# Kernel optimization log

Measured on AMD Instinct MI355X. Metric: run time of the kernel, lower is better.

The kernel has to match this reference:

```python
import jax, jax.numpy as jnp
import numpy as np

H, CM, CS = 8, 16, 32  # num_heads, hidden_mv_channels, hidden_s_channels
_INNER_IDX = np.array([0, 2, 3, 4, 8, 9, 10, 14])  # PGA multivector components without e0


def _make_basis():
    # 9 Pin(3,0,1)-equivariant linear maps on 16-dim multivectors:
    # 5 grade projections + 4 left-multiplications by e0 (grade k -> grade k+1 e0-blades).
    # Component order: [1, e0, e1, e2, e3, e01, e02, e03, e12, e13, e23, e012, e013, e023, e123, e0123]
    b = np.zeros((9, 16, 16), dtype=np.float32)
    grades = [[0], [1, 2, 3, 4], [5, 6, 7, 8, 9, 10], [11, 12, 13, 14], [15]]
    for k, idxs in enumerate(grades):
        for i in idxs:
            b[k, i, i] = 1.0
    e0maps = {5: [(0, 1)], 6: [(2, 5), (3, 6), (4, 7)], 7: [(8, 11), (9, 12), (10, 13)], 8: [(14, 15)]}
    for k, pairs in e0maps.items():
        for i, o in pairs:
            b[k, o, i] = 1.0
    return jnp.asarray(b)


BASIS = _make_basis()  # (9, 16_out_comp, 16_in_comp)


def equi_linear(mv, s, w_mv, w_s2mv, b_mv, w_mv2s, w_s2s, b_s):
    # mv: (..., c_in, 16); s: (..., s_in)
    out_mv = jnp.einsum('yai,ocy,...ci->...oa', BASIS, w_mv, mv)
    out_mv = out_mv.at[..., 0].add(jnp.einsum('...i,oi->...o', s, w_s2mv) + b_mv)
    out_s = (jnp.einsum('...c,sc->...s', mv[..., 0], w_mv2s)
             + jnp.einsum('...i,si->...s', s, w_s2s) + b_s)
    return out_mv, out_s


def reference(multivectors_kv, multivectors_q, scalars_kv, scalars_q,
              q_w_mv, q_w_s2mv, q_b_mv, q_w_mv2s, q_w_s2s, q_b_s,
              k_w_mv, k_w_s2mv, k_b_mv, k_w_mv2s, k_w_s2s, k_b_s,
              v_w_mv, v_w_s2mv, v_b_mv, v_w_mv2s, v_w_s2s, v_b_s,
              o_w_mv, o_w_s2mv, o_b_mv, o_w_mv2s, o_w_s2s, o_b_s):
    B, Q = multivectors_q.shape[0], multivectors_q.shape[1]
    q_mv, q_s = equi_linear(multivectors_q, scalars_q, q_w_mv, q_w_s2mv, q_b_mv, q_w_mv2s, q_w_s2s, q_b_s)
    k_mv, k_s = equi_linear(multivectors_kv, scalars_kv, k_w_mv, k_w_s2mv, k_b_mv, k_w_mv2s, k_w_s2s, k_b_s)
    v_mv, v_s = equi_linear(multivectors_kv, scalars_kv, v_w_mv, v_w_s2mv, v_b_mv, v_w_mv2s, v_w_s2s, v_b_s)
    # split heads; einops pattern '(hidden_channels num_heads)' => channel-major, head-minor
    q_mv = q_mv.reshape(B, Q, CM, H, 16).transpose(0, 3, 1, 2, 4)  # (B,H,Q,CM,16)
    q_s = q_s.reshape(B, Q, CS, H).transpose(0, 3, 1, 2)            # (B,H,Q,CS)
    # multi-query: single k/v head broadcast over H
    scale = 1.0 / jnp.sqrt(jnp.asarray(8 * CM + CS, dtype=q_mv.dtype))
    scores = (jnp.einsum('bhqcx,bkcx->bhqk', q_mv[..., _INNER_IDX], k_mv[..., _INNER_IDX])
              + jnp.einsum('bhqs,bks->bhqk', q_s, k_s)) * scale
    attn = jax.nn.softmax(scores, axis=-1)
    h_mv = jnp.einsum('bhqk,bkcx->bhqcx', attn, v_mv)
    h_s = jnp.einsum('bhqk,bkc->bhqc', attn, v_s)
    # merge heads; pattern '(n_heads hidden_channels)' => head-major
    h_mv = h_mv.transpose(0, 2, 1, 3, 4).reshape(B, Q, H * CM, 16)
    h_s = h_s.transpose(0, 2, 1, 3).reshape(B, Q, H * CS)
    out_mv, out_s = equi_linear(h_mv, h_s, o_w_mv, o_w_s2mv, o_b_mv, o_w_mv2s, o_w_s2s, o_b_s)
    return out_mv, out_s


def setup_inputs():
    key = jax.random.key(0)
    ks = jax.random.split(key, 32)
    B, NQ, NKV, IN_MV, IN_S = 4, 2048, 2048, 16, 32
    w = 0.05  # weight scale to keep attention logits sane

    def rn(k, shape, s=1.0):
        return jax.random.normal(k, shape, dtype=jnp.float32) * s

    return {
        'multivectors_kv': rn(ks[0], (B, NKV, IN_MV, 16)),
        'multivectors_q': rn(ks[1], (B, NQ, IN_MV, 16)),
        'scalars_kv': rn(ks[2], (B, NKV, IN_S)),
        'scalars_q': rn(ks[3], (B, NQ, IN_S)),
        'q_w_mv': rn(ks[4], (CM * H, IN_MV, 9), w),
        'q_w_s2mv': rn(ks[5], (CM * H, IN_S), w),
        'q_b_mv': jnp.zeros((CM * H,), jnp.float32),
        'q_w_mv2s': rn(ks[6], (CS * H, IN_MV), w),
        'q_w_s2s': rn(ks[7], (CS * H, IN_S), w),
        'q_b_s': jnp.zeros((CS * H,), jnp.float32),
        'k_w_mv': rn(ks[8], (CM, IN_MV, 9), w),
        'k_w_s2mv': rn(ks[9], (CM, IN_S), w),
        'k_b_mv': jnp.zeros((CM,), jnp.float32),
        'k_w_mv2s': rn(ks[10], (CS, IN_MV), w),
        'k_w_s2s': rn(ks[11], (CS, IN_S), w),
        'k_b_s': jnp.zeros((CS,), jnp.float32),
        'v_w_mv': rn(ks[12], (CM, IN_MV, 9), w),
        'v_w_s2mv': rn(ks[13], (CM, IN_S), w),
        'v_b_mv': jnp.zeros((CM,), jnp.float32),
        'v_w_mv2s': rn(ks[14], (CS, IN_MV), w),
        'v_w_s2s': rn(ks[15], (CS, IN_S), w),
        'v_b_s': jnp.zeros((CS,), jnp.float32),
        'o_w_mv': rn(ks[16], (16, CM * H, 9), w),
        'o_w_s2mv': rn(ks[17], (16, CS * H), w),
        'o_b_mv': jnp.zeros((16,), jnp.float32),
        'o_w_mv2s': rn(ks[18], (32, CM * H), w),
        'o_w_s2s': rn(ks[19], (32, CS * H), w),
        'o_b_s': jnp.zeros((32,), jnp.float32),
    }
```

## Files before the change

### kernel.cpp

```cpp
#include <hip/hip_runtime.h>
#include <hip/hip_bf16.h>
#include <math.h>

#define NB   4
#define NQL  2048
#define NKVL 2048
#define HN   8
#define DQK  160
#define DV   288
#define QT   256
#define KTL  64
#define KLP  168

#define SCALE 0.07905694150420949f

typedef __attribute__((ext_vector_type(8)))  short short8;
typedef __attribute__((ext_vector_type(4)))  float f32x4;
typedef __attribute__((ext_vector_type(16))) float f32x16;

__constant__ int c_grade[16] = {0,1,1,1,1,2,2,2,2,2,2,3,3,3,3,4};
__constant__ int c_inner[8]  = {0,2,3,4,8,9,10,14};
__constant__ int c_esrc[16]  = {-1,0,-1,-1,-1,2,3,4,-1,-1,-1,8,9,10,-1,14};
__constant__ int c_ey[16]    = {0,5,0,0,0,6,6,6,0,0,0,7,7,7,0,8};

__device__ __forceinline__ ushort f2bf(float v) {
  __hip_bfloat16 h = __float2bfloat16(v);
  union { __hip_bfloat16 b; ushort u; } cv; cv.b = h; return cv.u;
}

__device__ __forceinline__ void gload16(const void* g, void* l) {
  __builtin_amdgcn_global_load_lds(
      (const __attribute__((address_space(1))) unsigned int*)g,
      (__attribute__((address_space(3))) unsigned int*)l, 16, 0, 0);
}

#define KWMV   0
#define KS2MV  2304
#define KMV2S  2816
#define KS2S   3328
#define KBMV   4352
#define KBS    4368
#define VWMV   4400
#define VS2MV  6704
#define VMV2S  7216
#define VS2S   7728
#define VBMV   8752
#define VBS    8768
#define WLSZ   8800
#define XSTR   289
#define OSTR   456
#define KVPOS  8

__device__ __forceinline__ void kv_accum(const float* wL, const float* xL,
                                         int f, float acc[KVPOS]) {
  if (f < 160) {
    if (f < 128) {
      int c = f >> 3, a = c_inner[f & 7], y = c_grade[a];
      float bias = (a == 0) ? wL[KBMV + c] : 0.f;
#pragma unroll
      for (int p = 0; p < KVPOS; p++) acc[p] = bias;
      for (int ci = 0; ci < 16; ci++) {
        float w = wL[KWMV + (c*16 + ci)*9 + y];
#pragma unroll
        for (int p = 0; p < KVPOS; p++) acc[p] += w * xL[p*XSTR + ci*16 + a];
      }
      if (a == 0) {
        for (int i2 = 0; i2 < 32; i2++) {
          float w = wL[KS2MV + c*32 + i2];
#pragma unroll
          for (int p = 0; p < KVPOS; p++) acc[p] += w * xL[p*XSTR + 256 + i2];
        }
      }
    } else {
      int si = f - 128;
      float bias = wL[KBS + si];
#pragma unroll
      for (int p = 0; p < KVPOS; p++) acc[p] = bias;
      for (int ci = 0; ci < 16; ci++) {
        float w = wL[KMV2S + si*16 + ci];
#pragma unroll
        for (int p = 0; p < KVPOS; p++) acc[p] += w * xL[p*XSTR + ci*16];
      }
      for (int i2 = 0; i2 < 32; i2++) {
        float w = wL[KS2S + si*32 + i2];
#pragma unroll
        for (int p = 0; p < KVPOS; p++) acc[p] += w * xL[p*XSTR + 256 + i2];
      }
    }
  } else {
    int g = f - 160;
    if (g < 256) {
      int c = g >> 4, a = g & 15, y = c_grade[a];
      float bias = (a == 0) ? wL[VBMV + c] : 0.f;
#pragma unroll
      for (int p = 0; p < KVPOS; p++) acc[p] = bias;
      for (int ci = 0; ci < 16; ci++) {
        float w = wL[VWMV + (c*16 + ci)*9 + y];
#pragma unroll
        for (int p = 0; p < KVPOS; p++) acc[p] += w * xL[p*XSTR + ci*16 + a];
      }
      int sa = c_esrc[a];
      if (sa >= 0) {
        int ey = c_ey[a];
        for (int ci = 0; ci < 16; ci++) {
          float w = wL[VWMV + (c*16 + ci)*9 + ey];
#pragma unroll
          for (int p = 0; p < KVPOS; p++) acc[p] += w * xL[p*XSTR + ci*16 + sa];
        }
      }
      if (a == 0) {
        for (int i2 = 0; i2 < 32; i2++) {
          float w = wL[VS2MV + c*32 + i2];
#pragma unroll
          for (int p = 0; p < KVPOS; p++) acc[p] += w * xL[p*XSTR + 256 + i2];
        }
      }
    } else {
      int si = g - 256;
      float bias = wL[VBS + si];
#pragma unroll
      for (int p = 0; p < KVPOS; p++) acc[p] = bias;
      for (int ci = 0; ci < 16; ci++) {
        float w = wL[VMV2S + si*16 + ci];
#pragma unroll
        for (int p = 0; p < KVPOS; p++) acc[p] += w * xL[p*XSTR + ci*16];
      }
      for (int i2 = 0; i2 < 32; i2++) {
        float w = wL[VS2S + si*32 + i2];
#pragma unroll
        for (int p = 0; p < KVPOS; p++) acc[p] += w * xL[p*XSTR + 256 + i2];
      }
    }
  }
}

__global__ __launch_bounds__(256) void proj_kv_kernel(
    const float* __restrict__ mv_kv, const float* __restrict__ s_kv,
    const float* __restrict__ kw_mv, const float* __restrict__ kw_s2mv, const float* __restrict__ kb_mv,
    const float* __restrict__ kw_mv2s, const float* __restrict__ kw_s2s, const float* __restrict__ kb_s,
    const float* __restrict__ vw_mv, const float* __restrict__ vw_s2mv, const float* __restrict__ vb_mv,
    const float* __restrict__ vw_mv2s, const float* __restrict__ vw_s2s, const float* __restrict__ vb_s,
    ushort* __restrict__ Kf, ushort* __restrict__ VfT)
{
  __shared__ float wL[WLSZ];
  __shared__ float xL[KVPOS*XSTR];
  int t = threadIdx.x;
  for (int i = t; i < 2304; i += 256) wL[KWMV + i] = kw_mv[i];
  for (int i = t; i < 512;  i += 256) wL[KS2MV + i] = kw_s2mv[i];
  for (int i = t; i < 512;  i += 256) wL[KMV2S + i] = kw_mv2s[i];
  for (int i = t; i < 1024; i += 256) wL[KS2S + i] = kw_s2s[i];
  if (t < 16) wL[KBMV + t] = kb_mv[t];
  if (t < 32) wL[KBS + t] = kb_s[t];
  for (int i = t; i < 2304; i += 256) wL[VWMV + i] = vw_mv[i];
  for (int i = t; i < 512;  i += 256) wL[VS2MV + i] = vw_s2mv[i];
  for (int i = t; i < 512;  i += 256) wL[VMV2S + i] = vw_mv2s[i];
  for (int i = t; i < 1024; i += 256) wL[VS2S + i] = vw_s2s[i];
  if (t < 16) wL[VBMV + t] = vb_mv[t];
  if (t < 32) wL[VBS + t] = vb_s[t];

  int p0 = blockIdx.x * KVPOS;
  for (int i = t; i < KVPOS*256; i += 256) {
    int p = i >> 8, c = i & 255;
    xL[p*XSTR + c] = mv_kv[(size_t)(p0 + p)*256 + c];
  }
  if (t < KVPOS*32) {
    int p = t >> 5, c = t & 31;
    xL[p*XSTR + 256 + c] = s_kv[(size_t)(p0 + p)*32 + c];
  }
  __syncthreads();

  float acc0[KVPOS], acc1[KVPOS];
  kv_accum(wL, xL, t, acc0);
  if (t < 192) kv_accum(wL, xL, 256 + t, acc1);
  __syncthreads();

  ushort* oL = (ushort*)xL;
#pragma unroll
  for (int p = 0; p < KVPOS; p++) oL[p*OSTR + t] = f2bf(acc0[p]);
  if (t < 192) {
#pragma unroll
    for (int p = 0; p < KVPOS; p++) oL[p*OSTR + 256 + t] = f2bf(acc1[p]);
  }
  __syncthreads();

  int b = p0 >> 11, kv0 = p0 & 2047;
  for (int it = 0; it < 3; it++) {
    int j = t + it*256;
    if (j < KVPOS*80) {
      int p = j / 80, fp = j - p*80;
      uint u = (uint)oL[p*OSTR + 2*fp] | ((uint)oL[p*OSTR + 2*fp + 1] << 16);
      *(uint*)(Kf + (size_t)(p0 + p)*DQK + 2*fp) = u;
    }
  }
  for (int it = 0; it < 5; it++) {
    int j = t + it*256;
    if (j < DV*(KVPOS/2)) {
      int g = j >> 2, pp = j & 3;
      uint u = (uint)oL[(2*pp)*OSTR + 160 + g] | ((uint)oL[(2*pp+1)*OSTR + 160 + g] << 16);
      int kv = kv0 + 2*pp;
      int pos = (kv & ~63) + ((((kv >> 3) & 7) ^ (g & 7)) << 3) + (kv & 7);
      *(uint*)(VfT + ((size_t)b*DV + g)*NKVL + pos) = u;
    }
  }
}

#define OWT_SZ 34816
#define QWT_MV 0
#define QWT_S  20480
#define QBT    61440
#define QWT_SZ 62720
__global__ __launch_bounds__(256) void prep_w_kernel(
    const float* __restrict__ ow_mv, const float* __restrict__ ow_s2mv,
    const float* __restrict__ ow_mv2s, const float* __restrict__ ow_s2s,
    float* __restrict__ owT,
    const float* __restrict__ qw_mv, const float* __restrict__ qw_s2mv, const float* __restrict__ qb_mv,
    const float* __restrict__ qw_mv2s, const float* __restrict__ qw_s2s, const float* __restrict__ qb_s,
    float* __restrict__ qwT)
{
  int i = blockIdx.x*256 + threadIdx.x;
  if (i < OWT_SZ) {
    if (i < 18432) {
      int y = i / 2048, r = i & 2047, ch = r >> 4, o = r & 15;
      owT[i] = ow_mv[(size_t)(o*128 + ch)*9 + y];
    } else if (i < 22528) {
      int r = i - 18432, jj = r >> 4, o = r & 15;
      owT[i] = ow_s2mv[o*256 + jj];
    } else if (i < 26624) {
      int r = i - 22528, ch = r >> 5, si = r & 31;
      owT[i] = ow_mv2s[si*128 + ch];
    } else {
      int r = i - 26624, jj = r >> 5, si = r & 31;
      owT[i] = ow_s2s[si*256 + jj];
    }
    return;
  }
  int j = i - OWT_SZ;
  if (j >= QWT_SZ) return;
  if (j < QWT_S) {
    int ci = j / 1280, r = j - ci*1280, h = r / 160, f0 = r - h*160;
    float v;
    if (f0 < 128) {
      int c = f0 >> 3, a = c_inner[f0 & 7], y = c_grade[a];
      v = qw_mv[((c*HN + h)*16 + ci)*9 + y];
    } else {
      v = qw_mv2s[((f0 - 128)*HN + h)*16 + ci];
    }
    qwT[j] = v;
  } else if (j < QBT) {
    int k = j - QWT_S;
    int i2 = k / 1280, r = k - i2*1280, h = r / 160, f0 = r - h*160;
    float v;
    if (f0 < 128) {
      int c = f0 >> 3, a = c_inner[f0 & 7];
      v = (a == 0) ? qw_s2mv[(c*HN + h)*32 + i2] : 0.f;
    } else {
      v = qw_s2s[((f0 - 128)*HN + h)*32 + i2];
    }
    qwT[j] = v;
  } else {
    int r = j - QBT, h = r / 160, f0 = r - h*160;
    float v;
    if (f0 < 128) {
      int c = f0 >> 3, a = c_inner[f0 & 7];
      v = (a == 0) ? qb_mv[c*HN + h] : 0.f;
    } else {
      v = qb_s[(f0 - 128)*HN + h];
    }
    qwT[j] = v;
  }
}

#define QPOS 8
__global__ __launch_bounds__(320) void proj_q_kernel(
    const float* __restrict__ mv_q, const float* __restrict__ s_q,
    const float* __restrict__ qwT,
    ushort* __restrict__ Qf)
{
  __shared__ float xL[QPOS*XSTR];
  int t = threadIdx.x;
  int p0 = blockIdx.x * QPOS;
  for (int i = t; i < QPOS*256; i += 320) {
    int p = i >> 8, c = i & 255;
    xL[p*XSTR + c] = mv_q[(size_t)(p0 + p)*256 + c];
  }
  if (t < QPOS*32) {
    int p = t >> 5, c = t & 31;
    xL[p*XSTR + 256 + c] = s_q[(size_t)(p0 + p)*32 + c];
  }
  __syncthreads();

  int f0 = t % 160;
  int h0 = t / 160;
  int a = (f0 < 128) ? c_inner[f0 & 7] : 0;

  float acc[4][QPOS];
#pragma unroll
  for (int k = 0; k < 4; k++) {
    float bv = qwT[QBT + (h0 + 2*k)*160 + f0];
#pragma unroll
    for (int p = 0; p < QPOS; p++) acc[k][p] = bv;
  }
  for (int ci = 0; ci < 16; ci++) {
    float w0 = qwT[QWT_MV + (ci*HN + h0    )*160 + f0];
    float w1 = qwT[QWT_MV + (ci*HN + h0 + 2)*160 + f0];
    float w2 = qwT[QWT_MV + (ci*HN + h0 + 4)*160 + f0];
    float w3 = qwT[QWT_MV + (ci*HN + h0 + 6)*160 + f0];
#pragma unroll
    for (int p = 0; p < QPOS; p++) {
      float xv = xL[p*XSTR + ci*16 + a];
      acc[0][p] += w0*xv; acc[1][p] += w1*xv;
      acc[2][p] += w2*xv; acc[3][p] += w3*xv;
    }
  }
  for (int i2 = 0; i2 < 32; i2++) {
    float w0 = qwT[QWT_S + (i2*HN + h0    )*160 + f0];
    float w1 = qwT[QWT_S + (i2*HN + h0 + 2)*160 + f0];
    float w2 = qwT[QWT_S + (i2*HN + h0 + 4)*160 + f0];
    float w3 = qwT[QWT_S + (i2*HN + h0 + 6)*160 + f0];
#pragma unroll
    for (int p = 0; p < QPOS; p++) {
      float xv = xL[p*XSTR + 256 + i2];
      acc[0][p] += w0*xv; acc[1][p] += w1*xv;
      acc[2][p] += w2*xv; acc[3][p] += w3*xv;
    }
  }

  int b = p0 >> 11, q0 = p0 & 2047;
#pragma unroll
  for (int k = 0; k < 4; k++) {
    int h = h0 + 2*k;
    ushort* qdst = Qf + ((size_t)(b*HN + h)*NQL + q0)*DQK + f0;
#pragma unroll
    for (int p = 0; p < QPOS; p++)
      qdst[p*DQK] = f2bf(acc[k][p] * SCALE);
  }
}

__global__ __launch_bounds__(512, 2) void attn_kernel(
    const ushort* __restrict__ Kf,
    const ushort* __restrict__ VfT,
    const ushort* __restrict__ Qf,
    float* __restrict__ Hf)
{
  __shared__ ushort kL[2][KTL*KLP];
  __shared__ ushort vtL[2][DV*KTL];

  const int NT = NQL/QT;
  int bid = blockIdx.x;
  int swz = (bid & 7) * 32 + (bid >> 3);
  int bh = swz / NT;
  int qt = swz - bh*NT;
  int b = bh >> 3, h = bh & 7;
  int t = threadIdx.x, w = t >> 6, l = t & 63;
  int ql = l & 31, hb = l >> 5;

  const ushort* kb = Kf  + (size_t)b*NKVL*DQK;
  const ushort* vb = VfT + (size_t)b*DV*NKVL;

  const ushort* qrow = Qf + ((size_t)bh*NQL + (size_t)qt*QT + w*32 + ql)*DQK + hb*8;
  short8 qf[10];
#pragma unroll
  for (int ks = 0; ks < 10; ks++)
    qf[ks] = *(const short8*)(qrow + ks*16);

  f32x16 oA[9];
#pragma unroll
  for (int i = 0; i < 9; i++) oA[i] = (f32x16)(0.f);
  float m = -INFINITY, lsum = 0.f;

#define STAGE(KT, BUF) do {                                            \
    const ushort* kg_ = kb + (size_t)(KT)*KTL*DQK;                     \
    char* kd_ = (char*)&kL[BUF][0];                                    \
    for (int c_ = w; c_ < 21; c_ += 8) {                               \
      int off_ = c_*1024 + l*16;                                       \
      int row_ = off_ / 336;                                           \
      int bc_  = off_ - row_*336;                                      \
      const ushort* ga_ = kg_ + row_*DQK + ((bc_ < 320) ? (bc_ >> 1) : 0); \
      gload16(ga_, kd_ + c_*1024);                                     \
    }                                                                  \
    const ushort* vg_ = vb + (size_t)(KT)*KTL;                         \
    char* vd_ = (char*)&vtL[BUF][0];                                   \
    for (int c_ = w; c_ < 36; c_ += 8) {                               \
      int off_ = c_*1024 + l*16;                                       \
      int d_  = off_ >> 7;                                             \
      int bc_ = off_ & 127;                                            \
      const ushort* ga_ = vg_ + (size_t)d_*NKVL + (bc_ >> 1);          \
      gload16(ga_, vd_ + c_*1024);                                     \
    }                                                                  \
  } while (0)

  STAGE(0, 0);
  __syncthreads();

  for (int kt = 0; kt < NKVL/KTL; kt++) {
    int cur = kt & 1;
    if (kt + 1 < NKVL/KTL) STAGE(kt + 1, cur ^ 1);

    const ushort* kbuf  = &kL[cur][0];
    const ushort* vtbuf = &vtL[cur][0];

    f32x16 sA[2];
    __builtin_amdgcn_s_setprio(1);
#pragma unroll
    for (int kvb = 0; kvb < 2; kvb++) {
      sA[kvb] = (f32x16)(0.f);
      const ushort* krow = kbuf + (ql + 32*kvb)*KLP + hb*8;
#pragma unroll
      for (int ks = 0; ks < 10; ks++) {
        short8 kf = *(const short8*)(krow + ks*16);
        sA[kvb] = __builtin_amdgcn_mfma_f32_32x32x16_bf16(kf, qf[ks], sA[kvb], 0, 0, 0);
      }
    }
    __builtin_amdgcn_s_setprio(0);

    float tm = sA[0][0];
#pragma unroll
    for (int kvb = 0; kvb < 2; kvb++)
#pragma unroll
      for (int r = 0; r < 16; r++) tm = fmaxf(tm, sA[kvb][r]);
    tm = fmaxf(tm, __shfl_xor(tm, 32));
    if (!__all(tm - m <= 8.0f)) {
      float nm = fmaxf(m, tm);
      float ef = __expf(m - nm);
      lsum *= ef;
#pragma unroll
      for (int i = 0; i < 9; i++)
#pragma unroll
        for (int r = 0; r < 16; r++) oA[i][r] *= ef;
      m = nm;
    }
    float rs = 0.f;
#pragma unroll
    for (int kvb = 0; kvb < 2; kvb++)
#pragma unroll
      for (int r = 0; r < 16; r++) {
        float p = __expf(sA[kvb][r] - m);
        sA[kvb][r] = p;
        rs += p;
      }
    rs += __shfl_xor(rs, 32);
    lsum += rs;

    unsigned int pk[2][8];
#pragma unroll
    for (int kvb = 0; kvb < 2; kvb++)
#pragma unroll
      for (int k = 0; k < 8; k++) {
        unsigned int r_;
        asm("v_cvt_pk_bf16_f32 %0, %1, %2" : "=v"(r_) : "v"(sA[kvb][2*k]), "v"(sA[kvb][2*k+1]));
        pk[kvb][k] = r_;
      }

#pragma unroll
    for (int s = 0; s < 4; s++) {
      const int n0 = 2*s, n1 = 2*s + 1;
      unsigned int u[4];
#pragma unroll
      for (int p = 0; p < 4; p++) {
        unsigned int Xa = pk[n0 >> 2][(p & 1) + 2*(n0 & 3)];
        unsigned int Xb = pk[n1 >> 2][(p & 1) + 2*(n1 & 3)];
        int src = ql + 32*(p >> 1);
        unsigned int ua = __shfl((int)Xa, src);
        unsigned int ub = __shfl((int)Xb, src);
        u[p] = hb ? ub : ua;
      }
      union { unsigned int uu[4]; short8 s8; } pf;
      pf.uu[0] = u[0]; pf.uu[1] = u[1]; pf.uu[2] = u[2]; pf.uu[3] = u[3];
      __builtin_amdgcn_s_setprio(1);
#pragma unroll
      for (int db = 0; db < 9; db++) {
        int d = ql + 32*db;
        int col = (((2*s + hb) ^ (d & 7)) << 3);
        short8 vf = *(const short8*)(vtbuf + d*KTL + col);
        oA[db] = __builtin_amdgcn_mfma_f32_32x32x16_bf16(vf, pf.s8, oA[db], 0, 0, 0);
      }
      __builtin_amdgcn_s_setprio(0);
    }
    __syncthreads();
  }
#undef STAGE

  float inv = 1.0f / lsum;
  int q = qt*QT + w*32 + ql;
  float* orow = Hf + (((size_t)b*NQL + q)*HN + h)*DV;
#pragma unroll
  for (int db = 0; db < 9; db++)
#pragma unroll
    for (int j = 0; j < 4; j++) {
      int d0 = 32*db + 8*j + 4*hb;
      float4 st = make_float4(oA[db][4*j]*inv, oA[db][4*j+1]*inv,
                              oA[db][4*j+2]*inv, oA[db][4*j+3]*inv);
      *(float4*)(orow + d0) = st;
    }
}

#define HSTR2 2308
#define OPOS2 8
__global__ __launch_bounds__(512) void proj_o_kernel(
    const float* __restrict__ Hf,
    const float* __restrict__ owT,
    const float* __restrict__ ob_mv, const float* __restrict__ ob_s,
    float* __restrict__ outp)
{
  __shared__ float hL[OPOS2*HSTR2];
  __shared__ float pL[256*8];
  __shared__ float sP[8*48*8];
  int t = threadIdx.x;
  int p0 = blockIdx.x * OPOS2;
  for (int i = t; i < OPOS2*2304/4; i += 512) {
    int idx = i*4; int p = idx / 2304; int c = idx - p*2304;
    *(float4*)(hL + p*HSTR2 + c) = *(const float4*)(Hf + (size_t)(p0 + p)*2304 + c);
  }
  __syncthreads();

  const float* mvT   = owT;
  const float* s2mvT = owT + 18432;
  const float* mv2sT = owT + 22528;
  const float* s2sT  = owT + 26624;

  int o = t & 15, a = (t >> 4) & 15, seg = t >> 8;
  int oa = o*16 + a;
  int y = c_grade[a], sa = c_esrc[a], ey = c_ey[a];
  float acc[OPOS2];
#pragma unroll
  for (int p = 0; p < OPOS2; p++) acc[p] = 0.f;
  for (int ch = seg*64; ch < seg*64 + 64; ch++) {
    int xb = (ch >> 4)*288 + (ch & 15)*16;
    float w1 = mvT[y*2048 + ch*16 + o];
#pragma unroll
    for (int p = 0; p < OPOS2; p++) acc[p] += w1 * hL[p*HSTR2 + xb + a];
    if (sa >= 0) {
      float w2 = mvT[ey*2048 + ch*16 + o];
#pragma unroll
      for (int p = 0; p < OPOS2; p++) acc[p] += w2 * hL[p*HSTR2 + xb + sa];
    }
  }
  if (seg == 1) {
#pragma unroll
    for (int p = 0; p < OPOS2; p++) pL[oa*8 + p] = acc[p];
  }
  __syncthreads();
  if (seg == 0) {
#pragma unroll
    for (int p = 0; p < OPOS2; p++) acc[p] += pL[oa*8 + p];
  }

  int v = t >> 6, u = t & 63;
  float sacc[OPOS2];
#pragma unroll
  for (int p = 0; p < OPOS2; p++) sacc[p] = 0.f;
  if (u < 32) {
    int si = u;
    for (int ch = v*16; ch < v*16 + 16; ch++) {
      float w = mv2sT[ch*32 + si];
      int xb = (ch >> 4)*288 + (ch & 15)*16;
#pragma unroll
      for (int p = 0; p < OPOS2; p++) sacc[p] += w * hL[p*HSTR2 + xb];
    }
    for (int jj = v*32; jj < v*32 + 32; jj++) {
      float w = s2sT[jj*32 + si];
      int xb = (jj >> 5)*288 + 256 + (jj & 31);
#pragma unroll
      for (int p = 0; p < OPOS2; p++) sacc[p] += w * hL[p*HSTR2 + xb];
    }
  } else if (u < 48) {
    int o2 = u - 32;
    for (int jj = v*32; jj < v*32 + 32; jj++) {
      float w = s2mvT[jj*16 + o2];
      int xb = (jj >> 5)*288 + 256 + (jj & 31);
#pragma unroll
      for (int p = 0; p < OPOS2; p++) sacc[p] += w * hL[p*HSTR2 + xb];
    }
  }
  if (u < 48) {
#pragma unroll
    for (int p = 0; p < OPOS2; p++) sP[(v*48 + u)*8 + p] = sacc[p];
  }
  __syncthreads();

  if (seg == 0) {
    if (a == 0) {
      float bv = ob_mv[o];
#pragma unroll
      for (int p = 0; p < OPOS2; p++) {
        float s = bv;
#pragma unroll
        for (int vv = 0; vv < 8; vv++) s += sP[(vv*48 + 32 + o)*8 + p];
        acc[p] += s;
      }
    }
#pragma unroll
    for (int p = 0; p < OPOS2; p++) pL[oa*8 + p] = acc[p];
  }
  __syncthreads();
  for (int i = t; i < 256*OPOS2; i += 512) {
    int p = i >> 8, c = i & 255;
    outp[(size_t)(p0 + p)*256 + c] = pL[c*8 + p];
  }
  if (t >= 256 && t < 256 + 32) {
    int si = t - 256;
    float bv = ob_s[si];
    float* out_s = outp + (size_t)NB*NQL*256;
#pragma unroll
    for (int p = 0; p < OPOS2; p++) {
      float s = bv;
#pragma unroll
      for (int vv = 0; vv < 8; vv++) s += sP[(vv*48 + si)*8 + p];
      out_s[(size_t)(p0 + p)*32 + si] = s;
    }
  }
}

extern "C" void kernel_launch(void* const* d_in, const int* in_sizes, int n_in,
                              void* d_out, int out_size, void* d_ws, size_t ws_size,
                              hipStream_t stream)
{
  const float* mv_kv = (const float*)d_in[0];
  const float* mv_q  = (const float*)d_in[1];
  const float* s_kv  = (const float*)d_in[2];
  const float* s_q   = (const float*)d_in[3];

  ushort* Kf  = (ushort*)d_ws;
  ushort* VfT = Kf  + (size_t)NB*NKVL*DQK;
  ushort* Qf  = VfT + (size_t)NB*DV*NKVL;
  float*  Hf  = (float*)(Qf + (size_t)NB*HN*NQL*DQK);
  float*  owT = Hf + (size_t)NB*NQL*HN*DV;
  float*  qwT = owT + OWT_SZ;

  prep_w_kernel<<<(OWT_SZ + QWT_SZ + 255)/256, 256, 0, stream>>>(
      (const float*)d_in[22], (const float*)d_in[23],
      (const float*)d_in[25], (const float*)d_in[26], owT,
      (const float*)d_in[4], (const float*)d_in[5], (const float*)d_in[6],
      (const float*)d_in[7], (const float*)d_in[8], (const float*)d_in[9],
      qwT);
  proj_kv_kernel<<<NB*NKVL/KVPOS, 256, 0, stream>>>(mv_kv, s_kv,
      (const float*)d_in[10], (const float*)d_in[11], (const float*)d_in[12],
      (const float*)d_in[13], (const float*)d_in[14], (const float*)d_in[15],
      (const float*)d_in[16], (const float*)d_in[17], (const float*)d_in[18],
      (const float*)d_in[19], (const float*)d_in[20], (const float*)d_in[21],
      Kf, VfT);
  proj_q_kernel<<<NB*NQL/QPOS, 320, 0, stream>>>(mv_q, s_q, qwT, Qf);
  attn_kernel<<<NB*HN*(NQL/QT), 512, 0, stream>>>(Kf, VfT, Qf, Hf);
  proj_o_kernel<<<NB*NQL/OPOS2, 512, 0, stream>>>(Hf, owT,
      (const float*)d_in[24], (const float*)d_in[27],
      (float*)d_out);
}
```

Baseline: 335.2 us.

## Restructure output projection: fewer positions per block, float4 weight reuse per thread

The output projection kernel now handles 4 positions per 256-thread block instead of 8 per 512-thread block. Each thread computes 4 output channels using float4 weight loads, and the channel reduction is split into 4 segments reduced through padded shared memory. The goal is less LDS traffic per FMA, fewer redundant weight loads, and more blocks in flight thanks to a smaller shared-memory footprint. The cost is twice as many blocks, so weights are reloaded more often from cache, plus an extra shared-memory reduction pass.

Result: slower. 353.3 us (+5.4%).

```diff
diff --git a/kernel.cpp b/kernel.cpp
--- a/kernel.cpp
+++ b/kernel.cpp
@@ -495,19 +495,20 @@
 }
 
 #define HSTR2 2308
-#define OPOS2 8
-__global__ __launch_bounds__(512) void proj_o_kernel(
+#define OPOS3 4
+__global__ __launch_bounds__(256) void proj_o_kernel(
     const float* __restrict__ Hf,
     const float* __restrict__ owT,
     const float* __restrict__ ob_mv, const float* __restrict__ ob_s,
     float* __restrict__ outp)
 {
-  __shared__ float hL[OPOS2*HSTR2];
-  __shared__ float pL[256*8];
-  __shared__ float sP[8*48*8];
+  __shared__ float hL[OPOS3*HSTR2];
+  __shared__ float pL[4*64*17];
+  __shared__ float sP[4*48*5];
+  __shared__ float fL[256*5];
   int t = threadIdx.x;
-  int p0 = blockIdx.x * OPOS2;
-  for (int i = t; i < OPOS2*2304/4; i += 512) {
+  int p0 = blockIdx.x * OPOS3;
+  for (int i = t; i < OPOS3*2304/4; i += 256) {
     int idx = i*4; int p = idx / 2304; int c = idx - p*2304;
     *(float4*)(hL + p*HSTR2 + c) = *(const float4*)(Hf + (size_t)(p0 + p)*2304 + c);
   }
@@ -518,94 +519,112 @@
   const float* mv2sT = owT + 22528;
   const float* s2sT  = owT + 26624;
 
-  int o = t & 15, a = (t >> 4) & 15, seg = t >> 8;
-  int oa = o*16 + a;
+  int oq = t & 3, a = (t >> 2) & 15, seg = t >> 6;
   int y = c_grade[a], sa = c_esrc[a], ey = c_ey[a];
-  float acc[OPOS2];
-#pragma unroll
-  for (int p = 0; p < OPOS2; p++) acc[p] = 0.f;
-  for (int ch = seg*64; ch < seg*64 + 64; ch++) {
+  float acc[4][OPOS3];
+#pragma unroll
+  for (int j = 0; j < 4; j++)
+#pragma unroll
+    for (int p = 0; p < OPOS3; p++) acc[j][p] = 0.f;
+  for (int ch = seg*32; ch < seg*32 + 32; ch++) {
     int xb = (ch >> 4)*288 + (ch & 15)*16;
-    float w1 = mvT[y*2048 + ch*16 + o];
-#pragma unroll
-    for (int p = 0; p < OPOS2; p++) acc[p] += w1 * hL[p*HSTR2 + xb + a];
+    float4 w4 = *(const float4*)(mvT + y*2048 + ch*16 + oq*4);
+#pragma unroll
+    for (int p = 0; p < OPOS3; p++) {
+      float xa = hL[p*HSTR2 + xb + a];
+      acc[0][p] += w4.x*xa; acc[1][p] += w4.y*xa;
+      acc[2][p] += w4.z*xa; acc[3][p] += w4.w*xa;
+    }
     if (sa >= 0) {
-      float w2 = mvT[ey*2048 + ch*16 + o];
-#pragma unroll
-      for (int p = 0; p < OPOS2; p++) acc[p] += w2 * hL[p*HSTR2 + xb + sa];
-    }
-  }
-  if (seg == 1) {
-#pragma unroll
-    for (int p = 0; p < OPOS2; p++) pL[oa*8 + p] = acc[p];
-  }
-  __syncthreads();
-  if (seg == 0) {
-#pragma unroll
-    for (int p = 0; p < OPOS2; p++) acc[p] += pL[oa*8 + p];
+      float4 w4e = *(const float4*)(mvT + ey*2048 + ch*16 + oq*4);
+#pragma unroll
+      for (int p = 0; p < OPOS3; p++) {
+        float xs = hL[p*HSTR2 + xb + sa];
+        acc[0][p] += w4e.x*xs; acc[1][p] += w4e.y*xs;
+        acc[2][p] += w4e.z*xs; acc[3][p] += w4e.w*xs;
+      }
+    }
+  }
+  {
+    float* pd = pL + (seg*64 + oq*16 + a)*17;
+#pragma unroll
+    for (int j = 0; j < 4; j++)
+#pragma unroll
+      for (int p = 0; p < OPOS3; p++) pd[j*4 + p] = acc[j][p];
   }
 
   int v = t >> 6, u = t & 63;
-  float sacc[OPOS2];
-#pragma unroll
-  for (int p = 0; p < OPOS2; p++) sacc[p] = 0.f;
+  float sacc[OPOS3];
+#pragma unroll
+  for (int p = 0; p < OPOS3; p++) sacc[p] = 0.f;
   if (u < 32) {
     int si = u;
-    for (int ch = v*16; ch < v*16 + 16; ch++) {
+    for (int ch = v*32; ch < v*32 + 32; ch++) {
       float w = mv2sT[ch*32 + si];
       int xb = (ch >> 4)*288 + (ch & 15)*16;
 #pragma unroll
-      for (int p = 0; p < OPOS2; p++) sacc[p] += w * hL[p*HSTR2 + xb];
-    }
-    for (int jj = v*32; jj < v*32 + 32; jj++) {
+      for (int p = 0; p < OPOS3; p++) sacc[p] += w * hL[p*HSTR2 + xb];
+    }
+    for (int jj = v*64; jj < v*64 + 64; jj++) {
       float w = s2sT[jj*32 + si];
       int xb = (jj >> 5)*288 + 256 + (jj & 31);
 #pragma unroll
-      for (int p = 0; p < OPOS2; p++) sacc[p] += w * hL[p*HSTR2 + xb];
+      for (int p = 0; p < OPOS3; p++) sacc[p] += w * hL[p*HSTR2 + xb];
     }
   } else if (u < 48) {
     int o2 = u - 32;
-    for (int jj = v*32; jj < v*32 + 32; jj++) {
+    for (int jj = v*64; jj < v*64 + 64; jj++) {
       float w = s2mvT[jj*16 + o2];
       int xb = (jj >> 5)*288 + 256 + (jj & 31);
 #pragma unroll
-      for (int p = 0; p < OPOS2; p++) sacc[p] += w * hL[p*HSTR2 + xb];
+      for (int p = 0; p < OPOS3; p++) sacc[p] += w * hL[p*HSTR2 + xb];
     }
   }
   if (u < 48) {
 #pragma unroll
-    for (int p = 0; p < OPOS2; p++) sP[(v*48 + u)*8 + p] = sacc[p];
-  }
-  __syncthreads();
-
-  if (seg == 0) {
-    if (a == 0) {
+    for (int p = 0; p < OPOS3; p++) sP[(v*48 + u)*5 + p] = sacc[p];
+  }
+  __syncthreads();
+
+  {
+    int o = t >> 4, aa = t & 15;
+    float f[OPOS3];
+#pragma unroll
+    for (int p = 0; p < OPOS3; p++) f[p] = 0.f;
+#pragma unroll
+    for (int sg = 0; sg < 4; sg++) {
+      const float* pd = pL + (sg*64 + (o >> 2)*16 + aa)*17 + (o & 3)*4;
+#pragma unroll
+      for (int p = 0; p < OPOS3; p++) f[p] += pd[p];
+    }
+    if (aa == 0) {
       float bv = ob_mv[o];
 #pragma unroll
-      for (int p = 0; p < OPOS2; p++) {
+      for (int p = 0; p < OPOS3; p++) {
         float s = bv;
 #pragma unroll
-        for (int vv = 0; vv < 8; vv++) s += sP[(vv*48 + 32 + o)*8 + p];
-        acc[p] += s;
-      }
-    }
-#pragma unroll
-    for (int p = 0; p < OPOS2; p++) pL[oa*8 + p] = acc[p];
-  }
-  __syncthreads();
-  for (int i = t; i < 256*OPOS2; i += 512) {
+        for (int vv = 0; vv < 4; vv++) s += sP[(vv*48 + 32 + o)*5 + p];
+        f[p] += s;
+      }
+    }
+#pragma unroll
+    for (int p = 0; p < OPOS3; p++) fL[(o*16 + aa)*5 + p] = f[p];
+  }
+  __syncthreads();
+
+  for (int i = t; i < 256*OPOS3; i += 256) {
     int p = i >> 8, c = i & 255;
-    outp[(size_t)(p0 + p)*256 + c] = pL[c*8 + p];
-  }
-  if (t >= 256 && t < 256 + 32) {
-    int si = t - 256;
+    outp[(size_t)(p0 + p)*256 + c] = fL[c*5 + p];
+  }
+  if (t < 32) {
+    int si = t;
     float bv = ob_s[si];
     float* out_s = outp + (size_t)NB*NQL*256;
 #pragma unroll
-    for (int p = 0; p < OPOS2; p++) {
+    for (int p = 0; p < OPOS3; p++) {
       float s = bv;
 #pragma unroll
-      for (int vv = 0; vv < 8; vv++) s += sP[(vv*48 + si)*8 + p];
+      for (int vv = 0; vv < 4; vv++) s += sP[(vv*48 + si)*5 + p];
       out_s[(size_t)(p0 + p)*32 + si] = s;
     }
   }
@@ -641,7 +660,7 @@
       Kf, VfT);
   proj_q_kernel<<<NB*NQL/QPOS, 320, 0, stream>>>(mv_q, s_q, qwT, Qf);
   attn_kernel<<<NB*HN*(NQL/QT), 512, 0, stream>>>(Kf, VfT, Qf, Hf);
-  proj_o_kernel<<<NB*NQL/OPOS2, 512, 0, stream>>>(Hf, owT,
+  proj_o_kernel<<<NB*NQL/OPOS3, 256, 0, stream>>>(Hf, owT,
       (const float*)d_in[24], (const float*)d_in[27],
       (float*)d_out);
 }
```
